# Performance work log

Hardware: AMD Instinct MI355X
Metric: run time of the kernel (lower is better)

## Reference

```python
import jax, jax.numpy as jnp
import numpy as np

N_NODES = 100000
N_EDGES = 1000000
NHID = 128
N_CLASSES = 5000


def setup_inputs() -> dict:
    key = jax.random.key(0)
    ks = jax.random.split(key, 8)
    feature = jax.random.normal(ks[0], (N_NODES, NHID), dtype=jnp.float32)
    # Linear weights stored as [in, out] so forward is x @ W + b
    W1 = jax.random.normal(ks[1], (2 * NHID, NHID), dtype=jnp.float32) * (1.0 / np.sqrt(2 * NHID))
    b1 = jnp.zeros((NHID,), dtype=jnp.float32)
    alpha = jnp.full((NHID,), 0.25, dtype=jnp.float32)  # PReLU per-channel init
    W2 = jax.random.normal(ks[2], (NHID, 2), dtype=jnp.float32) * (1.0 / np.sqrt(NHID))
    b2 = jnp.zeros((2,), dtype=jnp.float32)
    row = jax.random.randint(ks[3], (N_EDGES,), 0, N_NODES, dtype=jnp.int64)
    col = jax.random.randint(ks[4], (N_EDGES,), 0, N_NODES, dtype=jnp.int64)
    label = jax.random.randint(ks[5], (N_NODES,), 0, N_CLASSES, dtype=jnp.int64)
    return {"feature": feature, "W1": W1, "b1": b1, "alpha": alpha,
            "W2": W2, "b2": b2, "row": row, "col": col, "label": label}


def reference(feature, W1, b1, alpha, W2, b2, row, col, label):
    # per-edge label: 1 if endpoints share a cluster label
    y = (label[row] == label[col]).astype(jnp.int32)  # [E]
    # edge gather + concat: [E, 2*nhid]
    x = jnp.concatenate([feature[row], feature[col]], axis=1)
    h = x @ W1 + b1                                   # [E, nhid]
    h = jnp.where(h >= 0, h, alpha * h)               # PReLU, per-channel alpha
    logits = h @ W2 + b2                              # [E, 2]
    logp = jax.nn.log_softmax(logits, axis=-1)
    # mean cross-entropy over edges
    loss = -jnp.mean(jnp.take_along_axis(logp, y[:, None], axis=1))
    return loss
```

## Files before the change

kernel.cpp:

```cpp
#include <hip/hip_runtime.h>
#include <hip/hip_bf16.h>

typedef __bf16 bf16_t;
typedef bf16_t bf16x8 __attribute__((ext_vector_type(8)));
typedef float floatx4 __attribute__((ext_vector_type(4)));
typedef float floatx2 __attribute__((ext_vector_type(2)));

#define N_NODES 100000
#define N_EDGES 1000000

#define BSHIFT 9
#define WIN 512
#define NBK 196
#define NBP 200
#define NSEG 6
#define SEGCAP 1024
#define BCAP (NSEG * SEGCAP)
#define SPCAP 16384
#define SCAT_BLKS 326
#define SCAT_WIN 3072

#define OFF_AUXR  12800000
#define OFF_AUXC  13600000
#define OFF_WT    14400000
#define OFF_WABS  14465536
#define OFF_W1G   14466048
#define OFF_CONST 14466560
#define OFF_RS    14466624ULL
#define OFF_SPILL 24297024ULL
#define OFF_CNT   24428096ULL
#define WS_NEED   24440960ULL
#define CNT_INTS  (NBP * 16 + 16)


__global__ __launch_bounds__(256) void k_prep(const float* __restrict__ W1,
                                              const float* __restrict__ b1,
                                              const float* __restrict__ alpha,
                                              const float* __restrict__ W2,
                                              const float* __restrict__ b2,
                                              bf16_t* __restrict__ WT,
                                              float* __restrict__ wabsp,
                                              float* __restrict__ w1g,
                                              float* __restrict__ constg,
                                              float* __restrict__ out,
                                              int* __restrict__ cnt,
                                              int zero_cnt) {
    const int t = threadIdx.x;
    if (blockIdx.x < 128) {
        int i = blockIdx.x * 256 + t;
        int n = i >> 7, k = i & 127;
        float v = (n < 128) ? W1[k * 128 + n] : W1[(k + 128) * 128 + (n - 128)];
        WT[i] = (bf16_t)v;
        return;
    }
    if (zero_cnt) {
        for (int i = t; i < CNT_INTS; i += 256) cnt[i] = 0;
    }
    __shared__ float w1L[128];
    if (t < 128) {
        float wd = W2[2 * t + 1] - W2[2 * t];
        float al = alpha[t];
        float w1v = wd * (1.f + al) * 0.5f;
        w1L[t] = w1v;
        w1g[t] = w1v;
        int col = (t & 64) + (t & 3) * 16 + ((t >> 2) & 15);
        float wdc = W2[2 * col + 1] - W2[2 * col];
        wabsp[t] = wdc * (1.f - alpha[col]) * 0.5f;
    }
    __syncthreads();
    if (t < 64) {
        float c = fmaf(w1L[t], b1[t], w1L[t + 64] * b1[t + 64]);
#pragma unroll
        for (int m = 32; m >= 1; m >>= 1) c += __shfl_xor(c, m, 64);
        if (t == 0) { *constg = c + (b2[1] - b2[0]); out[0] = 0.f; }
    }
}

__device__ inline unsigned fp4_code(float x) {
    float a = fabsf(x);
    unsigned code = (unsigned)(a > 0.25f) + (a > 0.75f) + (a > 1.25f) + (a > 1.75f)
                  + (a > 2.5f) + (a > 3.5f) + (a > 5.0f);
    return code | (x < 0.f ? 8u : 0u);
}

__global__ __launch_bounds__(256) void k_gemm(const float* __restrict__ F,
                                              const bf16_t* __restrict__ WT,
                                              const float* __restrict__ b1,
                                              const float* __restrict__ w1g,
                                              const int* __restrict__ label,
                                              unsigned char* __restrict__ PQ4,
                                              float2* __restrict__ auxR,
                                              float2* __restrict__ auxC,
                                              const int* __restrict__ row,
                                              const int* __restrict__ col,
                                              long long* __restrict__ RS,
                                              long long* __restrict__ spill,
                                              int* __restrict__ cnt,
                                              int do_scatter) {
    __shared__ __align__(16) char smem[34176];
    const int t = threadIdx.x;

    if (blockIdx.x < SCAT_BLKS) {
        if (!do_scatter) return;
        int* hist = (int*)smem;
        int* lofs = ((int*)smem) + NBP;
        int* base = ((int*)smem) + 2 * NBP;
        const int w0 = blockIdx.x * SCAT_WIN;
        for (int i = t; i < NBP; i += 256) { hist[i] = 0; lofs[i] = 0; }
        __syncthreads();
        int r[12], c[12];
#pragma unroll
        for (int k = 0; k < 12; ++k) {
            int e = w0 + k * 256 + t;
            int es = (e < N_EDGES) ? e : (N_EDGES - 1);
            r[k] = row[es]; c[k] = col[es];
            if (e < N_EDGES) atomicAdd(&hist[r[k] >> BSHIFT], 1);
        }
        __syncthreads();
        for (int b = t; b < NBP; b += 256) {
            int n = hist[b];
            base[b] = n ? atomicAdd(&cnt[b * 16], n) : 0;
        }
        __syncthreads();
#pragma unroll
        for (int k = 0; k < 12; ++k) {
            int e = w0 + k * 256 + t;
            if (e < N_EDGES) {
                int b = r[k] >> BSHIFT;
                int lo = atomicAdd(&lofs[b], 1);
                int gp = base[b] + lo;
                long long pk = (long long)(unsigned)r[k]
                             | ((long long)(unsigned)c[k] << 32);
                if (gp < BCAP) RS[(size_t)b * BCAP + gp] = pk;
                else {
                    int sp = atomicAdd(&cnt[NBP * 16], 1);
                    if (sp < SPCAP) spill[sp] = pk;
                }
            }
        }
        return;
    }

    bf16x8* Bs = (bf16x8*)smem;
    float (*sP1)[16] = (float (*)[16])(smem + 32768);
    float (*sP2)[16] = (float (*)[16])(smem + 33024);
    const int m0 = (blockIdx.x - SCAT_BLKS) * 32;

    const int w = t >> 6, lane = t & 63;
    const int l15 = lane & 15, quad = lane >> 4;
    const int rw = w >> 1, wq = w & 1;

    const int arow = m0 + rw * 16 + l15;
    const float4* Ar = (const float4*)(F + (size_t)arow * 128 + quad * 8);
    float4 fa[4], fb[4];
#pragma unroll
    for (int s = 0; s < 4; ++s) { fa[s] = Ar[s * 8]; fb[s] = Ar[s * 8 + 1]; }

    float w1v[4], bv[4];
#pragma unroll
    for (int nt = 0; nt < 4; ++nt) {
        int cch = wq * 64 + nt * 16 + l15;
        w1v[nt] = w1g[cch];
        bv[nt] = b1[cch];
    }

    const bf16x8* WT8 = (const bf16x8*)WT;
#pragma unroll
    for (int j = 0; j < 8; ++j) {
        int chunk = j * 256 + t;
        int cr = chunk >> 4, cc = chunk & 15;
        Bs[cr * 16 + (cc ^ (cr & 15))] = WT8[chunk];
    }

    bf16x8 Af[4];
#pragma unroll
    for (int s = 0; s < 4; ++s) {
        bf16x8 v;
        v[0] = (bf16_t)fa[s].x; v[1] = (bf16_t)fa[s].y;
        v[2] = (bf16_t)fa[s].z; v[3] = (bf16_t)fa[s].w;
        v[4] = (bf16_t)fb[s].x; v[5] = (bf16_t)fb[s].y;
        v[6] = (bf16_t)fb[s].z; v[7] = (bf16_t)fb[s].w;
        Af[s] = v;
    }
    __syncthreads();

#pragma unroll
    for (int h = 0; h < 2; ++h) {
        floatx4 acc[4] = {};
#pragma unroll
        for (int s = 0; s < 4; ++s) {
            bf16x8 Bf[4];
#pragma unroll
            for (int nt = 0; nt < 4; ++nt) {
                int cr = wq * 64 + nt * 16 + l15;
                Bf[nt] = Bs[cr * 16 + ((s * 4 + quad) ^ (cr & 15))];
            }
#pragma unroll
            for (int nt = 0; nt < 4; ++nt)
                acc[nt] = __builtin_amdgcn_mfma_f32_16x16x32_bf16(Af[s], Bf[nt], acc[nt], 0, 0, 0);
        }

#pragma unroll
        for (int rr = 0; rr < 4; ++rr) {
            float sv = 0.f;
#pragma unroll
            for (int nt = 0; nt < 4; ++nt) sv = fmaf(w1v[nt], acc[nt][rr], sv);
#pragma unroll
            for (int m = 8; m >= 1; m >>= 1) sv += __shfl_xor(sv, m, 64);
            if (l15 == 0) {
                if (h == 0) sP1[w][quad * 4 + rr] = sv;
                else        sP2[w][quad * 4 + rr] = sv;
            }
        }

#pragma unroll
        for (int rr = 0; rr < 4; ++rr) {
            int g = m0 + rw * 16 + quad * 4 + rr;
            float v0 = acc[0][rr], v1 = acc[1][rr], v2 = acc[2][rr], v3 = acc[3][rr];
            if (h == 0) { v0 += bv[0]; v1 += bv[1]; v2 += bv[2]; v3 += bv[3]; }
            unsigned pk = fp4_code(v0) | (fp4_code(v1) << 4)
                        | (fp4_code(v2) << 8) | (fp4_code(v3) << 12);
            *(unsigned short*)(PQ4 + (size_t)g * 128 + h * 64 + wq * 32 + l15 * 2) =
                (unsigned short)pk;
        }

        if (h == 0) {
            __syncthreads();
#pragma unroll
            for (int j = 0; j < 8; ++j) {
                int chunk = j * 256 + t;
                int cr = chunk >> 4, cc = chunk & 15;
                Bs[cr * 16 + (cc ^ (cr & 15))] = WT8[2048 + chunk];
            }
            __syncthreads();
        }
    }

    __syncthreads();
    if (t < 32) {
        int rw2 = t >> 4, ri = t & 15;
        float s1 = sP1[rw2 * 2][ri] + sP1[rw2 * 2 + 1][ri];
        float s2 = sP2[rw2 * 2][ri] + sP2[rw2 * 2 + 1][ri];
        int g = m0 + rw2 * 16 + ri;
        float lb = __int_as_float(label[g]);
        auxR[g] = make_float2(s1, lb);
        auxC[g] = make_float2(s2, lb);
    }
}

__device__ inline void fp4_decode(unsigned d, unsigned& pe, unsigned& po) {
    unsigned ne = d & 0x0F0F0F0Fu;
    unsigned no = (d >> 4) & 0x0F0F0F0Fu;
    pe = __builtin_amdgcn_perm(0x4C484440u, 0x3C383000u, ne & 0x07070707u)
       | ((ne & 0x08080808u) << 4);
    po = __builtin_amdgcn_perm(0x4C484440u, 0x3C383000u, no & 0x07070707u)
       | ((no & 0x08080808u) << 4);
}

template <int B>
__device__ inline float dw_pair(unsigned p, unsigned q, const float (&W)[32]) {
    unsigned pe, po, qe, qo;
    fp4_decode(p, pe, po);
    fp4_decode(q, qe, qo);
    floatx2 he0 = __builtin_amdgcn_cvt_pk_f32_fp8((int)pe, false)
                + __builtin_amdgcn_cvt_pk_f32_fp8((int)qe, false);
    floatx2 he1 = __builtin_amdgcn_cvt_pk_f32_fp8((int)pe, true)
                + __builtin_amdgcn_cvt_pk_f32_fp8((int)qe, true);
    floatx2 ho0 = __builtin_amdgcn_cvt_pk_f32_fp8((int)po, false)
                + __builtin_amdgcn_cvt_pk_f32_fp8((int)qo, false);
    floatx2 ho1 = __builtin_amdgcn_cvt_pk_f32_fp8((int)po, true)
                + __builtin_amdgcn_cvt_pk_f32_fp8((int)qo, true);
    float s;
    s = fabsf(he0[0]) * W[B + 0];
    s = fmaf(fabsf(he0[1]), W[B + 1], s);
    s = fmaf(fabsf(he1[0]), W[B + 2], s);
    s = fmaf(fabsf(he1[1]), W[B + 3], s);
    s = fmaf(fabsf(ho0[0]), W[B + 4], s);
    s = fmaf(fabsf(ho0[1]), W[B + 5], s);
    s = fmaf(fabsf(ho1[0]), W[B + 6], s);
    s = fmaf(fabsf(ho1[1]), W[B + 7], s);
    return s;
}

__device__ inline int2 ldRS(const long long* __restrict__ seg, int off,
                            int lane, int segN) {
    int ei = off + (lane >> 2);
    ei = (ei < segN) ? ei : (segN - 1);
    long long v = __builtin_nontemporal_load(&seg[ei]);
    return make_int2((int)(unsigned)(v & 0xFFFFFFFFll),
                     (int)(unsigned)((unsigned long long)v >> 32));
}

__device__ inline void ldGc(const unsigned char* __restrict__ PQ4,
                            const float2* __restrict__ auxC, int2 rc, int sub,
                            uint4& Q, float2& A) {
    Q = *(const uint4*)(PQ4 + (unsigned)rc.y * 128u + 64u + (unsigned)sub * 16u);
    A = make_float2(0.f, 0.f);
    if (sub & 1) A = auxC[rc.y];
}

__device__ inline float edge16s(const uint4* __restrict__ rowT,
                                const float2* __restrict__ auxT, int b0node,
                                int2 rc, uint4 Q, float2 Acol, int off,
                                int segN, int lane, int sub,
                                const float (&W)[32], float CB) {
    int rl = rc.x - b0node;
    uint4 P = rowT[rl * 4 + sub];
    float2 A = (sub & 1) ? Acol : auxT[rl];
    float s = dw_pair<0>(P.x, Q.x, W) + dw_pair<8>(P.y, Q.y, W)
            + dw_pair<16>(P.z, Q.z, W) + dw_pair<24>(P.w, Q.w, W);
    s += __shfl_xor(s, 1, 64);
    s += __shfl_xor(s, 2, 64);
    int gb = lane & ~3;
    float s2 = __shfl(A.x, gb + 1, 64);
    float lc = __shfl(A.y, gb + 1, 64);
    float D = A.x + s2 + CB + s;
    float sgn = (__float_as_int(A.y) == __float_as_int(lc)) ? -D : D;
    float loss = fmaxf(sgn, 0.f) + __logf(1.f + __expf(-fabsf(sgn)));
    bool valid = (sub == 0) && (off + (lane >> 2) < segN);
    return valid ? loss : 0.f;
}

__device__ inline void ldG(const unsigned char* __restrict__ PQ4,
                           const float2* __restrict__ auxR,
                           const float2* __restrict__ auxC, int2 rc, int sub,
                           uint4& P, uint4& Q, float2& A) {
    P = *(const uint4*)(PQ4 + (unsigned)rc.x * 128u + (unsigned)sub * 16u);
    Q = *(const uint4*)(PQ4 + (unsigned)rc.y * 128u + 64u + (unsigned)sub * 16u);
    A = (sub & 1) ? auxC[rc.y] : auxR[rc.x];
}

__device__ inline float edge16(uint4 P, uint4 Q, float2 A, int off, int segN,
                               int lane, int sub, const float (&W)[32],
                               float CB) {
    float s = dw_pair<0>(P.x, Q.x, W) + dw_pair<8>(P.y, Q.y, W)
            + dw_pair<16>(P.z, Q.z, W) + dw_pair<24>(P.w, Q.w, W);
    s += __shfl_xor(s, 1, 64);
    s += __shfl_xor(s, 2, 64);
    int gb = lane & ~3;
    float s2 = __shfl(A.x, gb + 1, 64);
    float lc = __shfl(A.y, gb + 1, 64);
    float D = A.x + s2 + CB + s;
    float sgn = (__float_as_int(A.y) == __float_as_int(lc)) ? -D : D;
    float loss = fmaxf(sgn, 0.f) + __logf(1.f + __expf(-fabsf(sgn)));
    bool valid = (sub == 0) && (off + (lane >> 2) < segN);
    return valid ? loss : 0.f;
}

__global__ __launch_bounds__(256) void k_edge_bkt(const unsigned char* __restrict__ PQ4,
                                                  const float2* __restrict__ auxRg,
                                                  const float2* __restrict__ auxCg,
                                                  const float* __restrict__ wabsp,
                                                  const float* __restrict__ constg,
                                                  const long long* __restrict__ RS,
                                                  const long long* __restrict__ spill,
                                                  const int* __restrict__ cnt,
                                                  float* __restrict__ out) {
    __shared__ __align__(16) unsigned char rowBytes[WIN * 64];
    __shared__ float2 auxT[WIN];
    __shared__ float sdata[4];
    const int t = threadIdx.x;
    const int lane = t & 63;
    const int w = t >> 6;
    const int sub = lane & 3;

    float W[32];
    const float* wb = wabsp + sub * 32;
#pragma unroll
    for (int d = 0; d < 4; ++d) {
        const float* wd = wb + d * 8;
        W[d * 8 + 0] = wd[0]; W[d * 8 + 1] = wd[2];
        W[d * 8 + 2] = wd[4]; W[d * 8 + 3] = wd[6];
        W[d * 8 + 4] = wd[1]; W[d * 8 + 5] = wd[3];
        W[d * 8 + 6] = wd[5]; W[d * 8 + 7] = wd[7];
    }
    const float CB = *constg;
    float accw = 0.f;

    const int blk = blockIdx.x;
    if (blk < NBP * NSEG) {
        const int bk = blk % NBP, sg = blk / NBP;
        int cc = cnt[bk * 16]; if (cc > BCAP) cc = BCAP;
        int st = sg * SEGCAP;
        int segN = cc - st; if (segN < 0) segN = 0; if (segN > SEGCAP) segN = SEGCAP;
        if (segN > 0) {
            const long long* seg = RS + (size_t)bk * BCAP + st;
            const int b0node = bk << BSHIFT;

            uint4* rowT = (uint4*)rowBytes;
            for (int c = t; c < WIN * 4; c += 256) {
                int node = c >> 2, part = c & 3;
                rowT[c] = *(const uint4*)(PQ4 + (size_t)(b0node + node) * 128
                                          + (unsigned)part * 16u);
            }
            for (int i = t; i < WIN; i += 256) auxT[i] = auxRg[b0node + i];
            __syncthreads();

            const int off0 = w * 16;
            const int nMy = (segN > off0) ? ((segN - off0 + 63) >> 6) : 0;
            if (nMy > 0) {
                int2 rc0 = ldRS(seg, off0, lane, segN);
                int2 rc1 = (nMy > 1) ? ldRS(seg, off0 + 64, lane, segN) : rc0;
                uint4 Q0; float2 A0;
                ldGc(PQ4, auxCg, rc0, sub, Q0, A0);
                for (int k = 0; k < nMy; ++k) {
                    int2 rc2 = (k + 2 < nMy) ? ldRS(seg, off0 + (k + 2) * 64, lane, segN)
                                             : rc0;
                    uint4 Q1; float2 A1;
                    int2 rcG = (k + 1 < nMy) ? rc1 : rc0;
                    ldGc(PQ4, auxCg, rcG, sub, Q1, A1);
                    __builtin_amdgcn_sched_barrier(0);
                    accw += edge16s((const uint4*)rowBytes, auxT, b0node, rc0,
                                    Q0, A0, off0 + k * 64, segN, lane, sub, W, CB);
                    rc0 = rc1; rc1 = rc2; Q0 = Q1; A0 = A1;
                }
            }
        }
    } else {
        int sc = cnt[NBP * 16]; if (sc > SPCAP) sc = SPCAP;
        int si = blk - NBP * NSEG;
        int per = (sc + 7) >> 3;
        int st = si * per;
        int segN = sc - st; if (segN < 0) segN = 0; if (segN > per) segN = per;
        const long long* seg = spill + st;
        const int off0 = w * 16;
        const int nMy = (segN > off0) ? ((segN - off0 + 63) >> 6) : 0;
        if (nMy > 0) {
            int2 rc0 = ldRS(seg, off0, lane, segN);
            int2 rc1 = (nMy > 1) ? ldRS(seg, off0 + 64, lane, segN) : rc0;
            uint4 P0, Q0; float2 A0;
            ldG(PQ4, auxRg, auxCg, rc0, sub, P0, Q0, A0);
            for (int k = 0; k < nMy; ++k) {
                int2 rc2 = (k + 2 < nMy) ? ldRS(seg, off0 + (k + 2) * 64, lane, segN)
                                         : rc0;
                uint4 P1, Q1; float2 A1;
                int2 rcG = (k + 1 < nMy) ? rc1 : rc0;
                ldG(PQ4, auxRg, auxCg, rcG, sub, P1, Q1, A1);
                __builtin_amdgcn_sched_barrier(0);
                accw += edge16(P0, Q0, A0, off0 + k * 64, segN, lane, sub, W, CB);
                rc0 = rc1; rc1 = rc2; P0 = P1; Q0 = Q1; A0 = A1;
            }
        }
    }

#pragma unroll
    for (int m = 32; m >= 1; m >>= 1) accw += __shfl_xor(accw, m, 64);
    if (lane == 0) sdata[w] = accw;
    __syncthreads();
    if (t == 0) {
        float ssum = (sdata[0] + sdata[1]) + (sdata[2] + sdata[3]);
        atomicAdd(out, ssum * (1.f / (float)N_EDGES));
    }
}

__global__ __launch_bounds__(256) void k_edge_loss(const unsigned char* __restrict__ PQ4,
                                                   const float2* __restrict__ auxR,
                                                   const float2* __restrict__ auxC,
                                                   const float* __restrict__ wabsp,
                                                   const float* __restrict__ constg,
                                                   const int* __restrict__ row,
                                                   const int* __restrict__ col,
                                                   float* __restrict__ out) {
    const int lane = threadIdx.x & 63;
    const int wid = (blockIdx.x * blockDim.x + threadIdx.x) >> 6;
    const int e0 = wid * 64;
    const int sub = lane & 3, eidx = lane >> 2;

    float W[32];
    const float* wb = wabsp + sub * 32;
#pragma unroll
    for (int d = 0; d < 4; ++d) {
        const float* wd = wb + d * 8;
        W[d * 8 + 0] = wd[0]; W[d * 8 + 1] = wd[2];
        W[d * 8 + 2] = wd[4]; W[d * 8 + 3] = wd[6];
        W[d * 8 + 4] = wd[1]; W[d * 8 + 5] = wd[3];
        W[d * 8 + 6] = wd[5]; W[d * 8 + 7] = wd[7];
    }
    const float CB = *constg;

    int el = e0 + lane;
    if (el >= N_EDGES) el = N_EDGES - 1;
    int rowreg = row[el];
    int colreg = col[el];

    int rV[4], cV[4];
#pragma unroll
    for (int c = 0; c < 4; ++c) {
        rV[c] = __shfl(rowreg, c * 16 + eidx, 64);
        cV[c] = __shfl(colreg, c * 16 + eidx, 64);
    }
    int alow = ((lane >> 5) << 4) + (lane & 15);
    int ra1 = __shfl(rowreg, alow, 64), ca1 = __shfl(colreg, alow, 64);
    int ra2 = __shfl(rowreg, 32 + alow, 64), ca2 = __shfl(colreg, 32 + alow, 64);
    float2 A1 = (lane & 16) ? auxC[ca1] : auxR[ra1];
    float2 A2 = (lane & 16) ? auxC[ca2] : auxR[ra2];

    uint4 P[4], Q[4];
#pragma unroll
    for (int c = 0; c < 4; ++c) {
        P[c] = *(const uint4*)(PQ4 + (unsigned)rV[c] * 128u + (unsigned)sub * 16u);
        Q[c] = *(const uint4*)(PQ4 + (unsigned)cV[c] * 128u + 64u + (unsigned)sub * 16u);
    }
    __builtin_amdgcn_sched_barrier(0);

    float acc = 0.f;
#pragma unroll
    for (int c = 0; c < 4; ++c) {
        float s = dw_pair<0>(P[c].x, Q[c].x, W)
                + dw_pair<8>(P[c].y, Q[c].y, W)
                + dw_pair<16>(P[c].z, Q[c].z, W)
                + dw_pair<24>(P[c].w, Q[c].w, W);
        s += __shfl_xor(s, 1, 64);
        s += __shfl_xor(s, 2, 64);
        const float2 Av = (c < 2) ? A1 : A2;
        const int base = (c & 1) * 32;
        float s1 = __shfl(Av.x, base + eidx, 64);
        float s2 = __shfl(Av.x, base + 16 + eidx, 64);
        float lr = __shfl(Av.y, base + eidx, 64);
        float lc = __shfl(Av.y, base + 16 + eidx, 64);
        float D = s1 + s2 + CB + s;
        float sgn = (__float_as_int(lr) == __float_as_int(lc)) ? -D : D;
        float loss = fmaxf(sgn, 0.f) + __logf(1.f + __expf(-fabsf(sgn)));
        int e = e0 + c * 16 + eidx;
        acc += (sub == 0 && e < N_EDGES) ? loss : 0.f;
    }

#pragma unroll
    for (int m = 32; m >= 1; m >>= 1) acc += __shfl_xor(acc, m, 64);
    __shared__ float sdata[4];
    int l64 = threadIdx.x & 63;
    int wv = threadIdx.x >> 6;
    if (l64 == 0) sdata[wv] = acc;
    __syncthreads();
    if (threadIdx.x == 0) {
        float ssum = (sdata[0] + sdata[1]) + (sdata[2] + sdata[3]);
        atomicAdd(out, ssum * (1.f / (float)N_EDGES));
    }
}

extern "C" void kernel_launch(void* const* d_in, const int* in_sizes, int n_in,
                              void* d_out, int out_size, void* d_ws, size_t ws_size,
                              hipStream_t stream) {
    const float* feature = (const float*)d_in[0];
    const float* W1      = (const float*)d_in[1];
    const float* b1      = (const float*)d_in[2];
    const float* alpha   = (const float*)d_in[3];
    const float* W2      = (const float*)d_in[4];
    const float* b2      = (const float*)d_in[5];
    const int*   row     = (const int*)d_in[6];
    const int*   col     = (const int*)d_in[7];
    const int*   label   = (const int*)d_in[8];
    float* out = (float*)d_out;

    char* ws = (char*)d_ws;
    unsigned char* PQ4 = (unsigned char*)(ws);
    float2* auxR = (float2*)(ws + OFF_AUXR);
    float2* auxC = (float2*)(ws + OFF_AUXC);
    bf16_t* WT   = (bf16_t*)(ws + OFF_WT);
    float* wabsp = (float*)(ws + OFF_WABS);
    float* w1g   = (float*)(ws + OFF_W1G);
    float* constg= (float*)(ws + OFF_CONST);

    const int bkt = (ws_size >= WS_NEED) ? 1 : 0;
    long long* RS    = (long long*)(ws + (bkt ? OFF_RS    : 0));
    long long* spill = (long long*)(ws + (bkt ? OFF_SPILL : 0));
    int*       cnt   = (int*)(ws + (bkt ? OFF_CNT    : 0));

    k_prep<<<129, 256, 0, stream>>>(W1, b1, alpha, W2, b2, WT, wabsp, w1g,
                                    constg, out, cnt, bkt);
    k_gemm<<<SCAT_BLKS + 3125, 256, 0, stream>>>(feature, WT, b1, w1g, label,
                                                 PQ4, auxR, auxC, row, col,
                                                 RS, spill, cnt, bkt);
    if (bkt) {
        k_edge_bkt<<<NBP * NSEG + 8, 256, 0, stream>>>(PQ4, auxR, auxC,
                                                       wabsp, constg, RS, spill,
                                                       cnt, out);
    } else {
        k_edge_loss<<<3907, 256, 0, stream>>>(PQ4, auxR, auxC, wabsp,
                                              constg, row, col, out);
    }
}
```

Baseline: 170.2 us.

## Halve GEMM weight LDS tile by loading weights in 64-column quarters

The node GEMM now stages the weight matrix in LDS in four 64-column chunks instead of two 128-column halves. This halves the shared-memory footprint per block, with the aim of fitting more blocks per CU, and reduces accumulator registers from four tiles to two. In exchange there are more __syncthreads barriers and LDS refills per block, and the packed FP4 output is written one byte at a time instead of as 16-bit stores. The output column interleave changes to match the new per-wave column assignment.

```diff
diff --git a/kernel.cpp b/kernel.cpp
--- a/kernel.cpp
+++ b/kernel.cpp
@@ -97,7 +97,7 @@
                                               long long* __restrict__ spill,
                                               int* __restrict__ cnt,
                                               int do_scatter) {
-    __shared__ __align__(16) char smem[34176];
+    __shared__ __align__(16) char smem[16896];
     const int t = threadIdx.x;
 
     if (blockIdx.x < SCAT_BLKS) {
@@ -142,13 +142,13 @@
     }
 
     bf16x8* Bs = (bf16x8*)smem;
-    float (*sP1)[16] = (float (*)[16])(smem + 32768);
-    float (*sP2)[16] = (float (*)[16])(smem + 33024);
+    float (*sP1)[16] = (float (*)[16])(smem + 16384);
+    float (*sP2)[16] = (float (*)[16])(smem + 16640);
     const int m0 = (blockIdx.x - SCAT_BLKS) * 32;
 
     const int w = t >> 6, lane = t & 63;
     const int l15 = lane & 15, quad = lane >> 4;
-    const int rw = w >> 1, wq = w & 1;
+    const int rw = w >> 1, cq = w & 1;
 
     const int arow = m0 + rw * 16 + l15;
     const float4* Ar = (const float4*)(F + (size_t)arow * 128 + quad * 8);
@@ -158,18 +158,10 @@
 
     float w1v[4], bv[4];
 #pragma unroll
-    for (int nt = 0; nt < 4; ++nt) {
-        int cch = wq * 64 + nt * 16 + l15;
-        w1v[nt] = w1g[cch];
-        bv[nt] = b1[cch];
-    }
-
-    const bf16x8* WT8 = (const bf16x8*)WT;
-#pragma unroll
-    for (int j = 0; j < 8; ++j) {
-        int chunk = j * 256 + t;
-        int cr = chunk >> 4, cc = chunk & 15;
-        Bs[cr * 16 + (cc ^ (cr & 15))] = WT8[chunk];
+    for (int j = 0; j < 4; ++j) {
+        int cch = (j >> 1) * 64 + cq * 32 + (j & 1) * 16 + l15;
+        w1v[j] = w1g[cch];
+        bv[j] = b1[cch];
     }
 
     bf16x8 Af[4];
@@ -182,57 +174,55 @@
         v[6] = (bf16_t)fb[s].z; v[7] = (bf16_t)fb[s].w;
         Af[s] = v;
     }
-    __syncthreads();
-
+
+    const bf16x8* WT8 = (const bf16x8*)WT;
 #pragma unroll
     for (int h = 0; h < 2; ++h) {
-        floatx4 acc[4] = {};
-#pragma unroll
-        for (int s = 0; s < 4; ++s) {
-            bf16x8 Bf[4];
-#pragma unroll
-            for (int nt = 0; nt < 4; ++nt) {
-                int cr = wq * 64 + nt * 16 + l15;
-                Bf[nt] = Bs[cr * 16 + ((s * 4 + quad) ^ (cr & 15))];
-            }
-#pragma unroll
-            for (int nt = 0; nt < 4; ++nt)
-                acc[nt] = __builtin_amdgcn_mfma_f32_16x16x32_bf16(Af[s], Bf[nt], acc[nt], 0, 0, 0);
-        }
-
+        float auxH[4] = {0.f, 0.f, 0.f, 0.f};
+#pragma unroll
+        for (int qq = 0; qq < 2; ++qq) {
+            __syncthreads();
+#pragma unroll
+            for (int i = 0; i < 4; ++i) {
+                int ch = i * 256 + t;
+                int cl = ch >> 4, cc = ch & 15;
+                Bs[cl * 16 + (cc ^ (cl & 15))] =
+                    WT8[(h * 128 + qq * 64 + cl) * 16 + cc];
+            }
+            __syncthreads();
+
+            floatx4 acc[2] = {};
+#pragma unroll
+            for (int s = 0; s < 4; ++s) {
+#pragma unroll
+                for (int nt = 0; nt < 2; ++nt) {
+                    int cl = cq * 32 + nt * 16 + l15;
+                    bf16x8 Bf = Bs[cl * 16 + ((s * 4 + quad) ^ (cl & 15))];
+                    acc[nt] = __builtin_amdgcn_mfma_f32_16x16x32_bf16(Af[s], Bf, acc[nt], 0, 0, 0);
+                }
+            }
+
+#pragma unroll
+            for (int rr = 0; rr < 4; ++rr) {
+                auxH[rr] = fmaf(w1v[qq * 2 + 0], acc[0][rr],
+                           fmaf(w1v[qq * 2 + 1], acc[1][rr], auxH[rr]));
+                int g = m0 + rw * 16 + quad * 4 + rr;
+                float v0 = acc[0][rr], v1 = acc[1][rr];
+                if (h == 0) { v0 += bv[qq * 2 + 0]; v1 += bv[qq * 2 + 1]; }
+                unsigned pk = fp4_code(v0) | (fp4_code(v1) << 4);
+                PQ4[(size_t)g * 128 + h * 64 + qq * 32 + l15 * 2 + cq] =
+                    (unsigned char)pk;
+            }
+        }
 #pragma unroll
         for (int rr = 0; rr < 4; ++rr) {
-            float sv = 0.f;
-#pragma unroll
-            for (int nt = 0; nt < 4; ++nt) sv = fmaf(w1v[nt], acc[nt][rr], sv);
+            float sv = auxH[rr];
 #pragma unroll
             for (int m = 8; m >= 1; m >>= 1) sv += __shfl_xor(sv, m, 64);
             if (l15 == 0) {
                 if (h == 0) sP1[w][quad * 4 + rr] = sv;
                 else        sP2[w][quad * 4 + rr] = sv;
             }
-        }
-
-#pragma unroll
-        for (int rr = 0; rr < 4; ++rr) {
-            int g = m0 + rw * 16 + quad * 4 + rr;
-            float v0 = acc[0][rr], v1 = acc[1][rr], v2 = acc[2][rr], v3 = acc[3][rr];
-            if (h == 0) { v0 += bv[0]; v1 += bv[1]; v2 += bv[2]; v3 += bv[3]; }
-            unsigned pk = fp4_code(v0) | (fp4_code(v1) << 4)
-                        | (fp4_code(v2) << 8) | (fp4_code(v3) << 12);
-            *(unsigned short*)(PQ4 + (size_t)g * 128 + h * 64 + wq * 32 + l15 * 2) =
-                (unsigned short)pk;
-        }
-
-        if (h == 0) {
-            __syncthreads();
-#pragma unroll
-            for (int j = 0; j < 8; ++j) {
-                int chunk = j * 256 + t;
-                int cr = chunk >> 4, cc = chunk & 15;
-                Bs[cr * 16 + (cc ^ (cr & 15))] = WT8[2048 + chunk];
-            }
-            __syncthreads();
         }
     }
 
```

Measured after the change: 172.5 us. Within noise of the previous version (+1.4%).
